# Performance work log

Measured on AMD Instinct MI355X. Metric: run time of the kernel, lower is better.

## Reference

```python
import jax, jax.numpy as jnp
import numpy as np

STRIDES = (8, 16, 32)
H = W = 640
SCORE_T = 0.5
NMS_T = 0.4


def setup_inputs() -> dict:
    key = jax.random.key(0)
    ks = jax.random.split(key, 9)
    feats = [(H // s) * (W // s) for s in STRIDES]  # 6400, 1600, 400
    d = {}
    for i, n in enumerate(feats):
        d[f"score{i}"] = jax.random.normal(ks[i], (1, n, 1), jnp.float32)
        d[f"bbox{i}"] = jax.random.normal(ks[3 + i], (1, n, 4), jnp.float32)
        d[f"kps{i}"] = jax.random.normal(ks[6 + i], (1, n, 10), jnp.float32)
    return d


def _anchors(stride):
    fh, fw = H // stride, W // stride
    yv, xv = jnp.meshgrid(jnp.arange(fh), jnp.arange(fw), indexing="ij")
    return jnp.stack([xv, yv], -1).reshape(-1, 2).astype(jnp.float32) * stride


def _decode(score, bbox, kps, stride):
    pts = _anchors(stride)                      # [N,2]
    s = jax.nn.sigmoid(score[0]).reshape(-1)    # [N]
    d = bbox[0] * stride                        # [N,4]
    x1 = pts[:, 0] - d[:, 0]
    y1 = pts[:, 1] - d[:, 1]
    x2 = pts[:, 0] + d[:, 2]
    y2 = pts[:, 1] + d[:, 3]
    b = jnp.stack([x1, y1, x2, y2], -1)         # [N,4]
    kd = (kps[0] * stride).reshape(-1, 5, 2)    # [N,5,2] (px,py pairs)
    k = (pts[:, None, :] + kd).reshape(-1, 10)  # [N,10]
    return s, b, k


def _iou(b):
    area = (b[:, 2] - b[:, 0]) * (b[:, 3] - b[:, 1])
    lt = jnp.maximum(b[:, None, :2], b[None, :, :2])
    rb = jnp.minimum(b[:, None, 2:], b[None, :, 2:])
    wh = jnp.clip(rb - lt, 0.0)
    inter = wh[..., 0] * wh[..., 1]
    return inter / (area[:, None] + area[None, :] - inter + 1e-9)


def _nms_keep(iou, valid, thresh):
    # greedy NMS on score-sorted boxes: keep i iff no earlier kept j has IoU>thresh
    n = valid.shape[0]
    def body(keep, xs):
        i, row = xs
        suppressed = jnp.any(keep & (row > thresh))
        keep = keep.at[i].set(valid[i] & ~suppressed)
        return keep, None
    keep, _ = jax.lax.scan(body, jnp.zeros(n, bool), (jnp.arange(n), iou))
    return keep


def reference(score0, score1, score2, bbox0, bbox1, bbox2, kps0, kps1, kps2):
    parts = [
        _decode(s, b, k, st)
        for s, b, k, st in zip(
            (score0, score1, score2), (bbox0, bbox1, bbox2), (kps0, kps1, kps2), STRIDES
        )
    ]
    scores = jnp.concatenate([p[0] for p in parts])  # [8400]
    boxes = jnp.concatenate([p[1] for p in parts])   # [8400,4]
    kpss = jnp.concatenate([p[2] for p in parts])    # [8400,10]
    order = jnp.argsort(-scores)                     # score-descending (NMS order)
    scores = scores[order]
    boxes = boxes[order]
    kpss = kpss[order]
    valid = scores > SCORE_T                         # threshold mask
    iou = _iou(jax.lax.stop_gradient(boxes))         # [8400,8400] ~282MB
    keep = _nms_keep(iou, valid, NMS_T)
    m = keep.astype(boxes.dtype)
    # fixed-shape equivalent of dynamic gather: suppressed rows zeroed, keep mask returned
    return boxes * m[:, None], scores * m, kpss * m[:, None], keep
```

## Files before the change

### kernel.cpp

```cpp
#include <hip/hip_runtime.h>
#include <math.h>

#define N_TOT 8400
#define MASK_WORDS 132
#define CAP 32
#define RT 33

typedef unsigned long long u64;

__device__ __forceinline__ unsigned mono_u32(float f) {
    unsigned u = __float_as_uint(f);
    return (u & 0x80000000u) ? ~u : (u | 0x80000000u);
}

__global__ void decode_kernel(const float* __restrict__ score0, const float* __restrict__ bbox0, const float* __restrict__ kps0,
                              const float* __restrict__ score1, const float* __restrict__ bbox1, const float* __restrict__ kps1,
                              const float* __restrict__ score2, const float* __restrict__ bbox2, const float* __restrict__ kps2,
                              float* __restrict__ logit, float* __restrict__ sig,
                              float* __restrict__ box, float* __restrict__ kps,
                              u64* __restrict__ key, int* __restrict__ rank,
                              unsigned int* __restrict__ cnt,
                              u64* __restrict__ validw, u64* __restrict__ rowflag) {
    int i = blockIdx.x * blockDim.x + threadIdx.x;
    if (i >= N_TOT) return;
    if (i < MASK_WORDS) { validw[i] = 0ull; rowflag[i] = 0ull; }
    rank[i] = 0;
    cnt[i] = 0u;
    const float *sc, *bb, *kp;
    int m, F; float s;
    if (i < 6400)      { sc = score0; bb = bbox0; kp = kps0; m = i;        F = 80; s = 8.f;  }
    else if (i < 8000) { sc = score1; bb = bbox1; kp = kps1; m = i - 6400; F = 40; s = 16.f; }
    else               { sc = score2; bb = bbox2; kp = kps2; m = i - 8000; F = 20; s = 32.f; }
    float px = (float)(m % F) * s;
    float py = (float)(m / F) * s;
    float lg = sc[m];
    logit[i] = lg;
    sig[i] = 1.0f / (1.0f + expf(-lg));
    key[i] = ((u64)(~mono_u32(lg)) << 14) | (u64)i;
    float d0 = bb[m*4+0]*s, d1 = bb[m*4+1]*s, d2 = bb[m*4+2]*s, d3 = bb[m*4+3]*s;
    box[i*4+0] = px - d0;
    box[i*4+1] = py - d1;
    box[i*4+2] = px + d2;
    box[i*4+3] = py + d3;
    #pragma unroll
    for (int c = 0; c < 5; ++c) {
        kps[i*10 + 2*c]   = px + kp[m*10 + 2*c]   * s;
        kps[i*10 + 2*c+1] = py + kp[m*10 + 2*c+1] * s;
    }
}

__global__ __launch_bounds__(256) void rank_kernel(const u64* __restrict__ key, int* __restrict__ rank) {
    __shared__ u64 tile[256];
    int i = blockIdx.x * 256 + threadIdx.x;
    int t0 = blockIdx.y * 256;
    u64 ki = (i < N_TOT) ? key[i] : 0ull;
    int j = t0 + threadIdx.x;
    tile[threadIdx.x] = (j < N_TOT) ? key[j] : ~0ull;
    __syncthreads();
    if (i >= N_TOT) return;
    int rk = 0;
    #pragma unroll 8
    for (int k = 0; k < 256; ++k) {
        rk += (tile[k] < ki) ? 1 : 0;
    }
    if (rk) atomicAdd(&rank[i], rk);
}

__global__ void scatter_kernel(const int* __restrict__ rank,
                               const float* __restrict__ logit, const float* __restrict__ sig,
                               const float* __restrict__ box, const float* __restrict__ kps,
                               float* __restrict__ s_logit, float* __restrict__ s_sig,
                               float* __restrict__ s_box, float* __restrict__ s_kps,
                               u64* __restrict__ validw) {
    int i = blockIdx.x * blockDim.x + threadIdx.x;
    if (i >= N_TOT) return;
    int r = rank[i];
    float lg = logit[i];
    s_logit[r] = lg;
    s_sig[r] = sig[i];
    #pragma unroll
    for (int c = 0; c < 4; ++c)  s_box[r*4+c] = box[i*4+c];
    #pragma unroll
    for (int c = 0; c < 10; ++c) s_kps[r*10+c] = kps[i*10+c];
    if (lg > 0.f) atomicOr(&validw[r >> 6], 1ull << (r & 63));
}

__global__ __launch_bounds__(64) void pairs_kernel(const float* __restrict__ s_logit,
                                                   const float* __restrict__ s_box,
                                                   unsigned int* __restrict__ cnt,
                                                   ulonglong2* __restrict__ ent,
                                                   u64* __restrict__ rowflag) {
    int x = blockIdx.x;
    int y = blockIdx.y;
    int rb, cw;
    if (x + y < MASK_WORDS) { rb = x; cw = x + y; }
    else {
        if (y == MASK_WORDS / 2) return;
        rb = x + y - MASK_WORDS; cw = x;
    }
    int tid = threadIdx.x;

    __shared__ float4 cbox[64];
    __shared__ float  carea[64];
    int j0 = cw * 64;
    int j = j0 + tid;
    float4 cb = make_float4(0.f, 0.f, 0.f, 0.f);
    float lgj = -1.f;
    if (j < N_TOT) {
        cb = ((const float4*)s_box)[j];
        lgj = s_logit[j];
    }
    cbox[tid] = cb;
    carea[tid] = (cb.z - cb.x) * (cb.w - cb.y);
    u64 cvalid = __ballot(j < N_TOT && lgj > 0.f);
    __syncthreads();
    if (cvalid == 0ull) return;

    int r = rb * 64 + tid;
    float lgr = (r < N_TOT) ? s_logit[r] : -1.f;
    if (__ballot(lgr > 0.f) == 0ull) return;

    u64 bits = 0ull;
    if (lgr > 0.f) {
        float4 rb4 = ((const float4*)s_box)[r];
        float rarea = (rb4.z - rb4.x) * (rb4.w - rb4.y);
        #pragma unroll 4
        for (int k = 0; k < 64; ++k) {
            float4 c4 = cbox[k];
            float ltx = fmaxf(rb4.x, c4.x);
            float lty = fmaxf(rb4.y, c4.y);
            float rbx = fminf(rb4.z, c4.z);
            float rby = fminf(rb4.w, c4.w);
            float w = fmaxf(rbx - ltx, 0.f);
            float h = fmaxf(rby - lty, 0.f);
            float inter = w * h;
            float iou = inter / (rarea + carea[k] - inter + 1e-9f);
            bits |= (iou > 0.4f) ? (1ull << k) : 0ull;
        }
        u64 m = cvalid;
        if (cw == rb) m &= (tid == 63) ? 0ull : (~0ull << (tid + 1));
        bits &= m;
    }
    if (bits) {
        unsigned idx = atomicAdd(&cnt[r], 1u);
        if (idx < CAP) {
            ulonglong2 e; e.x = bits; e.y = (u64)cw;
            ent[(size_t)r * CAP + idx] = e;
        }
        atomicOr(&rowflag[r >> 6], 1ull << (r & 63));
    }
}

__global__ __launch_bounds__(64) void nms_kernel(const u64* __restrict__ rowflag_g,
                                                 const u64* __restrict__ validw_g,
                                                 const unsigned int* __restrict__ cnt_g,
                                                 const ulonglong2* __restrict__ ent_g,
                                                 u64* __restrict__ keep_words) {
    __shared__ u64 rem_lds[MASK_WORDS];
    __shared__ unsigned short wlist[MASK_WORDS];
    int lane = threadIdx.x;

    u64 rf[3], vw[3];
    #pragma unroll
    for (int s = 0; s < 3; ++s) {
        int w = s * 64 + lane;
        rf[s] = (w < MASK_WORDS) ? rowflag_g[w] : 0ull;
        vw[s] = (w < MASK_WORDS) ? validw_g[w] : 0ull;
        if (w < MASK_WORDS) rem_lds[w] = 0ull;
    }

    int base = 0;
    #pragma unroll
    for (int s = 0; s < 3; ++s) {
        bool nz = rf[s] != 0ull;
        u64 bal = __ballot(nz);
        int pos = __popcll(bal & ((1ull << lane) - 1ull));
        if (nz) wlist[base + pos] = (unsigned short)(s * 64 + lane);
        base += (int)__popcll(bal);
    }
    int n_w = base;
    __syncthreads();

    auto LOADW = [&](int t, int &wd, unsigned &c, ulonglong2 &e0, ulonglong2 &e1, u64 &lb) {
        wd = 0; c = 0u; e0.x = 0ull; e0.y = 0ull; e1.x = 0ull; e1.y = 0ull; lb = 0ull;
        if (t < n_w) {
            wd = (int)wlist[t];
            int row = wd * 64 + lane;
            if (row < N_TOT) {
                c = cnt_g[row];
                if (c > 0u) { e0 = ent_g[(size_t)row * CAP];     if ((int)e0.y == wd) lb |= e0.x; }
                if (c > 1u) { e1 = ent_g[(size_t)row * CAP + 1]; if ((int)e1.y == wd) lb |= e1.x; }
                if (c > 2u) {
                    unsigned cm = min(c, (unsigned)CAP);
                    for (unsigned e = 2; e < cm; ++e) {
                        ulonglong2 g = ent_g[(size_t)row * CAP + e];
                        if ((int)g.y == wd) lb |= g.x;
                    }
                }
            }
        }
    };

    int wA, wB; unsigned cA, cB; ulonglong2 eA0, eA1, eB0, eB1; u64 lbA, lbB;
    LOADW(0, wA, cA, eA0, eA1, lbA);
    LOADW(1, wB, cB, eB0, eB1, lbB);

    for (int t = 0; t < n_w; ++t) {
        int wC; unsigned cC; ulonglong2 eC0, eC1; u64 lbC;
        LOADW(t + 2, wC, cC, eC0, eC1, lbC);

        __syncthreads();
        u64 remw = rem_lds[wA];
        u64 cand = __ballot(cA > 0u) & ~remw;
        if (cand) {
            u64 kept;
            u64 localmask = __ballot(lbA != 0ull) & cand;
            if (localmask == 0ull) {
                kept = cand;
            } else {
                kept = 0ull;
                u64 remw_new = remw;
                u64 pend = cand;
                while (pend) {
                    int b = __builtin_ctzll(pend);
                    pend &= pend - 1ull;
                    if (!((remw_new >> b) & 1ull)) {
                        kept |= 1ull << b;
                        unsigned lo = (unsigned)__builtin_amdgcn_readlane((int)(unsigned)lbA, b);
                        unsigned hi = (unsigned)__builtin_amdgcn_readlane((int)(unsigned)(lbA >> 32), b);
                        remw_new |= ((u64)hi << 32) | (u64)lo;
                        pend &= ~remw_new;
                    }
                }
                if (lane == 0) rem_lds[wA] = remw_new;
            }
            if ((kept >> lane) & 1ull) {
                if (cA > 0u) { int yw = (int)eA0.y; if (yw != wA) atomicOr(&rem_lds[yw], eA0.x); }
                if (cA > 1u) { int yw = (int)eA1.y; if (yw != wA) atomicOr(&rem_lds[yw], eA1.x); }
                if (cA > 2u) {
                    unsigned cm = min(cA, (unsigned)CAP);
                    int row = wA * 64 + lane;
                    for (unsigned e = 2; e < cm; ++e) {
                        ulonglong2 g = ent_g[(size_t)row * CAP + e];
                        int yw = (int)g.y;
                        if (yw != wA) atomicOr(&rem_lds[yw], g.x);
                    }
                }
            }
        }
        wA = wB; cA = cB; eA0 = eB0; eA1 = eB1; lbA = lbB;
        wB = wC; cB = cC; eB0 = eC0; eB1 = eC1; lbB = lbC;
    }

    __syncthreads();
    #pragma unroll
    for (int s = 0; s < 3; ++s) {
        int w = s * 64 + lane;
        if (w < MASK_WORDS) keep_words[w] = vw[s] & ~rem_lds[w];
    }
}

__global__ void output_kernel(const float* __restrict__ s_sig, const float* __restrict__ s_box,
                              const float* __restrict__ s_kps,
                              const u64* __restrict__ keep_words,
                              float* __restrict__ out) {
    int r = blockIdx.x * blockDim.x + threadIdx.x;
    if (r >= N_TOT) return;
    float m = ((keep_words[r >> 6] >> (r & 63)) & 1ull) ? 1.0f : 0.0f;
    float* ob = out;
    float* os = out + 33600;
    float* okp = out + 42000;
    float* om = out + 126000;
    #pragma unroll
    for (int c = 0; c < 4; ++c)  ob[r*4+c] = s_box[r*4+c] * m;
    os[r] = s_sig[r] * m;
    #pragma unroll
    for (int c = 0; c < 10; ++c) okp[r*10+c] = s_kps[r*10+c] * m;
    om[r] = m;
}

extern "C" void kernel_launch(void* const* d_in, const int* in_sizes, int n_in,
                              void* d_out, int out_size, void* d_ws, size_t ws_size,
                              hipStream_t stream) {
    const float *score0, *bbox0, *kps0, *score1, *bbox1, *kps1, *score2, *bbox2, *kps2;
    if (in_sizes[1] == 25600) {
        score0 = (const float*)d_in[0]; bbox0 = (const float*)d_in[1]; kps0 = (const float*)d_in[2];
        score1 = (const float*)d_in[3]; bbox1 = (const float*)d_in[4]; kps1 = (const float*)d_in[5];
        score2 = (const float*)d_in[6]; bbox2 = (const float*)d_in[7]; kps2 = (const float*)d_in[8];
    } else {
        score0 = (const float*)d_in[0]; score1 = (const float*)d_in[1]; score2 = (const float*)d_in[2];
        bbox0  = (const float*)d_in[3]; bbox1  = (const float*)d_in[4]; bbox2  = (const float*)d_in[5];
        kps0   = (const float*)d_in[6]; kps1   = (const float*)d_in[7]; kps2   = (const float*)d_in[8];
    }

    char* ws = (char*)d_ws;
    float* logit   = (float*)(ws + 0);
    float* sig     = (float*)(ws + 33600);
    float* box     = (float*)(ws + 67200);
    float* kps     = (float*)(ws + 201600);
    int*   rank    = (int*)  (ws + 537600);
    float* s_logit = (float*)(ws + 571200);
    float* s_sig   = (float*)(ws + 604800);
    float* s_box   = (float*)(ws + 638400);
    float* s_kps   = (float*)(ws + 772800);
    u64*   keep_words = (u64*)(ws + 1108800);
    u64*   validw     = (u64*)(ws + 1110144);
    u64*   rowflag    = (u64*)(ws + 1111296);
    unsigned int* cnt = (unsigned int*)(ws + 1112448);
    u64*   key        = (u64*)(ws + 1146368);
    ulonglong2*   ent = (ulonglong2*)(ws + 1213568);

    float* out = (float*)d_out;

    decode_kernel<<<(N_TOT + 255) / 256, 256, 0, stream>>>(
        score0, bbox0, kps0, score1, bbox1, kps1, score2, bbox2, kps2,
        logit, sig, box, kps, key, rank, cnt, validw, rowflag);
    rank_kernel<<<dim3(RT, RT), 256, 0, stream>>>(key, rank);
    scatter_kernel<<<33, 256, 0, stream>>>(rank, logit, sig, box, kps,
                                           s_logit, s_sig, s_box, s_kps, validw);
    pairs_kernel<<<dim3(MASK_WORDS, MASK_WORDS / 2 + 1), 64, 0, stream>>>(s_logit, s_box, cnt, ent, rowflag);
    nms_kernel<<<1, 64, 0, stream>>>(rowflag, validw, cnt, ent, keep_words);
    output_kernel<<<33, 256, 0, stream>>>(s_sig, s_box, s_kps, keep_words, out);
}
```

Measured before the change: 113.5 us.

## Store diagonal IoU masks separately and deepen NMS prefetch pipeline

The pairs kernel now writes each diagonal block's intra-word suppression mask to a dedicated per-row array, so these masks no longer go through the entry list. The single-wave NMS kernel reads that diagonal mask directly, prefetches three words ahead with four entries each unconditionally, and drops the per-iteration barriers. The local greedy loop now only walks rows that have intra-word suppressors. This shortens the serial critical path of the one-block NMS. The cost is more speculative loads and an extra workspace buffer. Removing the barriers relies on wave-synchronous LDS ordering within a single 64-lane block. The __syncthreads after cbox/carea are filled in the pairs kernel is also removed. With several waves per block that would be a race, but at 64 threads (a single wave) it is probably fine.

```diff
diff --git a/kernel.cpp b/kernel.cpp
--- a/kernel.cpp
+++ b/kernel.cpp
@@ -60,9 +60,7 @@
     if (i >= N_TOT) return;
     int rk = 0;
     #pragma unroll 8
-    for (int k = 0; k < 256; ++k) {
-        rk += (tile[k] < ki) ? 1 : 0;
-    }
+    for (int k = 0; k < 256; ++k) rk += (tile[k] < ki) ? 1 : 0;
     if (rk) atomicAdd(&rank[i], rk);
 }
 
@@ -89,6 +87,7 @@
                                                    const float* __restrict__ s_box,
                                                    unsigned int* __restrict__ cnt,
                                                    ulonglong2* __restrict__ ent,
+                                                   u64* __restrict__ diag,
                                                    u64* __restrict__ rowflag) {
     int x = blockIdx.x;
     int y = blockIdx.y;
@@ -98,12 +97,12 @@
         if (y == MASK_WORDS / 2) return;
         rb = x + y - MASK_WORDS; cw = x;
     }
+    bool isdiag = (rb == cw);
     int tid = threadIdx.x;
 
     __shared__ float4 cbox[64];
     __shared__ float  carea[64];
-    int j0 = cw * 64;
-    int j = j0 + tid;
+    int j = cw * 64 + tid;
     float4 cb = make_float4(0.f, 0.f, 0.f, 0.f);
     float lgj = -1.f;
     if (j < N_TOT) {
@@ -113,16 +112,15 @@
     cbox[tid] = cb;
     carea[tid] = (cb.z - cb.x) * (cb.w - cb.y);
     u64 cvalid = __ballot(j < N_TOT && lgj > 0.f);
-    __syncthreads();
-    if (cvalid == 0ull) return;
+    if (!isdiag && cvalid == 0ull) return;
 
     int r = rb * 64 + tid;
-    float lgr = (r < N_TOT) ? s_logit[r] : -1.f;
-    if (__ballot(lgr > 0.f) == 0ull) return;
+    float lgr = isdiag ? lgj : ((r < N_TOT) ? s_logit[r] : -1.f);
+    if (!isdiag && __ballot(lgr > 0.f) == 0ull) return;
 
     u64 bits = 0ull;
-    if (lgr > 0.f) {
-        float4 rb4 = ((const float4*)s_box)[r];
+    if (cvalid != 0ull && lgr > 0.f) {
+        float4 rb4 = isdiag ? cb : ((const float4*)s_box)[r];
         float rarea = (rb4.z - rb4.x) * (rb4.w - rb4.y);
         #pragma unroll 4
         for (int k = 0; k < 64; ++k) {
@@ -138,8 +136,13 @@
             bits |= (iou > 0.4f) ? (1ull << k) : 0ull;
         }
         u64 m = cvalid;
-        if (cw == rb) m &= (tid == 63) ? 0ull : (~0ull << (tid + 1));
+        if (isdiag) m &= (tid == 63) ? 0ull : (~0ull << (tid + 1));
         bits &= m;
+    }
+    if (isdiag) {
+        if (r < N_TOT) diag[r] = bits;
+        if (bits) atomicOr(&rowflag[r >> 6], 1ull << (r & 63));
+        return;
     }
     if (bits) {
         unsigned idx = atomicAdd(&cnt[r], 1u);
@@ -154,6 +157,7 @@
 __global__ __launch_bounds__(64) void nms_kernel(const u64* __restrict__ rowflag_g,
                                                  const u64* __restrict__ validw_g,
                                                  const unsigned int* __restrict__ cnt_g,
+                                                 const u64* __restrict__ diag_g,
                                                  const ulonglong2* __restrict__ ent_g,
                                                  u64* __restrict__ keep_words) {
     __shared__ u64 rem_lds[MASK_WORDS];
@@ -179,80 +183,90 @@
         base += (int)__popcll(bal);
     }
     int n_w = base;
-    __syncthreads();
-
-    auto LOADW = [&](int t, int &wd, unsigned &c, ulonglong2 &e0, ulonglong2 &e1, u64 &lb) {
-        wd = 0; c = 0u; e0.x = 0ull; e0.y = 0ull; e1.x = 0ull; e1.y = 0ull; lb = 0ull;
-        if (t < n_w) {
-            wd = (int)wlist[t];
-            int row = wd * 64 + lane;
-            if (row < N_TOT) {
-                c = cnt_g[row];
-                if (c > 0u) { e0 = ent_g[(size_t)row * CAP];     if ((int)e0.y == wd) lb |= e0.x; }
-                if (c > 1u) { e1 = ent_g[(size_t)row * CAP + 1]; if ((int)e1.y == wd) lb |= e1.x; }
-                if (c > 2u) {
-                    unsigned cm = min(c, (unsigned)CAP);
-                    for (unsigned e = 2; e < cm; ++e) {
-                        ulonglong2 g = ent_g[(size_t)row * CAP + e];
-                        if ((int)g.y == wd) lb |= g.x;
-                    }
-                }
-            }
+
+    int wdA=0, wdB=0, wdC=0;
+    unsigned cA=0u, cB=0u, cC=0u;
+    u64 lbA=0ull, lbB=0ull, lbC=0ull;
+    ulonglong2 A0,A1,A2,A3, B0,B1,B2,B3, C0,C1,C2,C3;
+    A0.x=A0.y=0ull; A1=A0; A2=A0; A3=A0;
+    B0=A0; B1=A0; B2=A0; B3=A0; C0=A0; C1=A0; C2=A0; C3=A0;
+
+#define LOADST(t, wd, c, lb, e0, e1, e2, e3) do {              \
+        wd = 0; c = 0u; lb = 0ull;                             \
+        if ((t) < n_w) {                                       \
+            wd = (int)wlist[t];                                \
+            int row_ = wd * 64 + lane;                         \
+            if (row_ < N_TOT) {                                \
+                const ulonglong2* ep_ = ent_g + (size_t)row_ * CAP; \
+                c  = cnt_g[row_];                              \
+                lb = diag_g[row_];                             \
+                e0 = ep_[0];                                   \
+                e1 = ep_[1];                                   \
+                e2 = ep_[2];                                   \
+                e3 = ep_[3];                                   \
+            }                                                  \
+        }                                                      \
+    } while (0)
+
+#define STEP(wd, c, lb, e0, e1, e2, e3, TNEXT) do {            \
+        u64 remw = rem_lds[wd];                                \
+        u64 cand = __ballot(c > 0u || lb != 0ull) & ~remw;     \
+        if (cand) {                                            \
+            u64 kept;                                          \
+            u64 S = __ballot(lb != 0ull) & cand;               \
+            if (S == 0ull) {                                   \
+                kept = cand;                                   \
+            } else {                                           \
+                u64 rn = remw;                                 \
+                u64 pend = S;                                  \
+                while (pend) {                                 \
+                    int b_ = __builtin_ctzll(pend);            \
+                    pend &= pend - 1ull;                       \
+                    if (!((rn >> b_) & 1ull)) {                \
+                        unsigned lo_ = (unsigned)__builtin_amdgcn_readlane((int)(unsigned)lb, b_); \
+                        unsigned hi_ = (unsigned)__builtin_amdgcn_readlane((int)(unsigned)(lb >> 32), b_); \
+                        rn |= ((u64)hi_ << 32) | (u64)lo_;     \
+                        pend &= ~rn;                           \
+                    }                                          \
+                }                                              \
+                kept = cand & ~rn;                             \
+                if (lane == 0) rem_lds[wd] = rn;               \
+            }                                                  \
+            bool kp_ = (kept >> lane) & 1ull;                  \
+            if (kp_) {                                         \
+                if (c > 0u) atomicOr(&rem_lds[(int)e0.y], e0.x); \
+                if (c > 1u) atomicOr(&rem_lds[(int)e1.y], e1.x); \
+                if (c > 2u) atomicOr(&rem_lds[(int)e2.y], e2.x); \
+                if (c > 3u) atomicOr(&rem_lds[(int)e3.y], e3.x); \
+            }                                                  \
+            if (__ballot(kp_ && c > 4u)) {                     \
+                if (kp_ && c > 4u) {                           \
+                    unsigned cm_ = min(c, (unsigned)CAP);      \
+                    int row_ = wd * 64 + lane;                 \
+                    for (unsigned e_ = 4; e_ < cm_; ++e_) {    \
+                        ulonglong2 g_ = ent_g[(size_t)row_ * CAP + e_]; \
+                        atomicOr(&rem_lds[(int)g_.y], g_.x);   \
+                    }                                          \
+                }                                              \
+            }                                                  \
+        }                                                      \
+        LOADST(TNEXT, wd, c, lb, e0, e1, e2, e3);              \
+    } while (0)
+
+    if (n_w > 0) {
+        LOADST(0, wdA, cA, lbA, A0, A1, A2, A3);
+        LOADST(1, wdB, cB, lbB, B0, B1, B2, B3);
+        LOADST(2, wdC, cC, lbC, C0, C1, C2, C3);
+        int t = 0;
+        while (true) {
+            STEP(wdA, cA, lbA, A0, A1, A2, A3, t + 3); if (++t >= n_w) break;
+            STEP(wdB, cB, lbB, B0, B1, B2, B3, t + 3); if (++t >= n_w) break;
+            STEP(wdC, cC, lbC, C0, C1, C2, C3, t + 3); if (++t >= n_w) break;
         }
-    };
-
-    int wA, wB; unsigned cA, cB; ulonglong2 eA0, eA1, eB0, eB1; u64 lbA, lbB;
-    LOADW(0, wA, cA, eA0, eA1, lbA);
-    LOADW(1, wB, cB, eB0, eB1, lbB);
-
-    for (int t = 0; t < n_w; ++t) {
-        int wC; unsigned cC; ulonglong2 eC0, eC1; u64 lbC;
-        LOADW(t + 2, wC, cC, eC0, eC1, lbC);
-
-        __syncthreads();
-        u64 remw = rem_lds[wA];
-        u64 cand = __ballot(cA > 0u) & ~remw;
-        if (cand) {
-            u64 kept;
-            u64 localmask = __ballot(lbA != 0ull) & cand;
-            if (localmask == 0ull) {
-                kept = cand;
-            } else {
-                kept = 0ull;
-                u64 remw_new = remw;
-                u64 pend = cand;
-                while (pend) {
-                    int b = __builtin_ctzll(pend);
-                    pend &= pend - 1ull;
-                    if (!((remw_new >> b) & 1ull)) {
-                        kept |= 1ull << b;
-                        unsigned lo = (unsigned)__builtin_amdgcn_readlane((int)(unsigned)lbA, b);
-                        unsigned hi = (unsigned)__builtin_amdgcn_readlane((int)(unsigned)(lbA >> 32), b);
-                        remw_new |= ((u64)hi << 32) | (u64)lo;
-                        pend &= ~remw_new;
-                    }
-                }
-                if (lane == 0) rem_lds[wA] = remw_new;
-            }
-            if ((kept >> lane) & 1ull) {
-                if (cA > 0u) { int yw = (int)eA0.y; if (yw != wA) atomicOr(&rem_lds[yw], eA0.x); }
-                if (cA > 1u) { int yw = (int)eA1.y; if (yw != wA) atomicOr(&rem_lds[yw], eA1.x); }
-                if (cA > 2u) {
-                    unsigned cm = min(cA, (unsigned)CAP);
-                    int row = wA * 64 + lane;
-                    for (unsigned e = 2; e < cm; ++e) {
-                        ulonglong2 g = ent_g[(size_t)row * CAP + e];
-                        int yw = (int)g.y;
-                        if (yw != wA) atomicOr(&rem_lds[yw], g.x);
-                    }
-                }
-            }
-        }
-        wA = wB; cA = cB; eA0 = eB0; eA1 = eB1; lbA = lbB;
-        wB = wC; cB = cC; eB0 = eC0; eB1 = eC1; lbB = lbC;
-    }
-
-    __syncthreads();
+    }
+#undef STEP
+#undef LOADST
+
     #pragma unroll
     for (int s = 0; s < 3; ++s) {
         int w = s * 64 + lane;
@@ -309,6 +323,7 @@
     unsigned int* cnt = (unsigned int*)(ws + 1112448);
     u64*   key        = (u64*)(ws + 1146368);
     ulonglong2*   ent = (ulonglong2*)(ws + 1213568);
+    u64*   diag       = (u64*)(ws + 5514368);
 
     float* out = (float*)d_out;
 
@@ -318,7 +333,8 @@
     rank_kernel<<<dim3(RT, RT), 256, 0, stream>>>(key, rank);
     scatter_kernel<<<33, 256, 0, stream>>>(rank, logit, sig, box, kps,
                                            s_logit, s_sig, s_box, s_kps, validw);
-    pairs_kernel<<<dim3(MASK_WORDS, MASK_WORDS / 2 + 1), 64, 0, stream>>>(s_logit, s_box, cnt, ent, rowflag);
-    nms_kernel<<<1, 64, 0, stream>>>(rowflag, validw, cnt, ent, keep_words);
+    pairs_kernel<<<dim3(MASK_WORDS, MASK_WORDS / 2 + 1), 64, 0, stream>>>(
+        s_logit, s_box, cnt, ent, diag, rowflag);
+    nms_kernel<<<1, 64, 0, stream>>>(rowflag, validw, cnt, diag, ent, keep_words);
     output_kernel<<<33, 256, 0, stream>>>(s_sig, s_box, s_kps, keep_words, out);
 }
```

Result: no change. 111.3 us (-1.9%).
